# Kernel optimization log

Hardware: AMD Instinct MI355X
Metric: run time of the kernel (lower is better)

## Reference

```python
import jax, jax.numpy as jnp
import numpy as np

B, IN, OUT = 131072, 512, 512


def setup_inputs() -> dict:
    key = jax.random.key(0)
    k1, k2 = jax.random.split(key)
    x = jax.random.normal(k1, (B, IN), dtype=jnp.float32)
    # matches reset_parameters: normal(0, sqrt(1/in_features))
    weight = jax.random.normal(k2, (OUT, IN), dtype=jnp.float32) * jnp.sqrt(1.0 / IN)
    bias = jnp.zeros((OUT,), dtype=jnp.float32)
    return {"x": x, "weight": weight, "bias": bias}


def _binarize(w):
    # deterministic sign binarization: w >= 0 -> +1, else -1
    return jnp.where(w >= 0, 1.0, -1.0).astype(w.dtype)


def reference(x, weight, bias):
    wb = _binarize(weight)            # [out, in], values in {-1, +1}
    # out = x @ wb.T + bias           # [B, out]
    return jnp.einsum("bi,oi->bo", x, wb) + bias
```

## Files before the change

kernel.cpp:

```cpp
#include <hip/hip_runtime.h>
#include <stdint.h>


#define BATCH   131072
#define IN_F    512
#define OUT_F   512
#define BM      64
#define NKT     32

using f32x4  = __attribute__((ext_vector_type(4))) float;
using f32x16 = __attribute__((ext_vector_type(16))) float;
using short8 = __attribute__((ext_vector_type(8))) short;
using usv8   = __attribute__((ext_vector_type(8))) unsigned short;
using u32    = uint32_t;

__global__ void prep_w(const float* __restrict__ W, unsigned short* __restrict__ wf) {
    int t = blockIdx.x * blockDim.x + threadIdx.x;
    int l  = t & 63;
    int nf = (t >> 6) & 15;
    int kt = t >> 10;
    int n = nf * 32 + (l & 31);
    int k = kt * 16 + ((l >> 5) << 3);
    const float* src = W + (size_t)n * IN_F + k;
    f32x4 w0 = *(const f32x4*)(src);
    f32x4 w1 = *(const f32x4*)(src + 4);
    usv8 o;
#pragma unroll
    for (int j = 0; j < 4; ++j) {
        o[j]     = (w0[j] >= 0.0f) ? 0x3F80u : 0xBF80u;
        o[j + 4] = (w1[j] >= 0.0f) ? 0x3F80u : 0xBF80u;
    }
    *(usv8*)(wf + (size_t)t * 8) = o;
}

__global__ __launch_bounds__(512, 4) void gemm_bin(
    const float* __restrict__ X, const unsigned short* __restrict__ WF,
    const float* __restrict__ bias, float* __restrict__ out) {

    __shared__ __align__(16) unsigned short lds[BM * IN_F];

    const int tid  = threadIdx.x;
    const int lane = tid & 63;
    const int wv   = tid >> 6;
    const int m0   = blockIdx.x * BM;

    {
        const int r  = tid >> 3;
        const int sg = tid & 7;
        const float* xr = X + (size_t)(m0 + r) * IN_F;
        char* lrow = (char*)lds + r * 1024;
        const int swz = (r & 7) << 4;
#pragma unroll
        for (int p = 0; p < 8; ++p) {
            const int f0 = sg * 8 + p * 64;
            f32x4 a = *(const f32x4*)(xr + f0);
            f32x4 b = *(const f32x4*)(xr + f0 + 4);
            u32 w0, w1, w2, w3;
            asm("v_cvt_pk_bf16_f32 %0, %1, %2" : "=v"(w0) : "v"(a[0]), "v"(a[1]));
            asm("v_cvt_pk_bf16_f32 %0, %1, %2" : "=v"(w1) : "v"(a[2]), "v"(a[3]));
            asm("v_cvt_pk_bf16_f32 %0, %1, %2" : "=v"(w2) : "v"(b[0]), "v"(b[1]));
            asm("v_cvt_pk_bf16_f32 %0, %1, %2" : "=v"(w3) : "v"(b[2]), "v"(b[3]));
            union { u32 w[4]; usv8 v; } pk;
            pk.w[0] = w0; pk.w[1] = w1; pk.w[2] = w2; pk.w[3] = w3;
            *(usv8*)(lrow + ((sg * 16 + p * 128) ^ swz)) = pk.v;
        }
    }

    f32x16 acc[2][2];
#pragma unroll
    for (int fn = 0; fn < 2; ++fn) {
        const float bv = bias[wv * 64 + fn * 32 + (lane & 31)];
#pragma unroll
        for (int rg = 0; rg < 2; ++rg)
#pragma unroll
            for (int r = 0; r < 16; ++r) acc[rg][fn][r] = bv;
    }
    __syncthreads();

    const int arow  = (lane & 31) * 1024;
    const int ak4   = (lane >> 5) << 4;
    const int aswz  = (lane & 7) << 4;
    const char* lptr = (const char*)lds;
    const short8* wb = (const short8*)(WF) + ((size_t)(wv * 2) * 64 + lane);

#define LDA(dst, kt_)                                                          \
    {                                                                          \
        const int koff_ = ((kt_) * 32 + ak4) ^ aswz;                           \
        _Pragma("unroll")                                                      \
        for (int rg = 0; rg < 2; ++rg)                                         \
            dst[rg] = *(const short8*)(lptr + rg * 32768 + arow + koff_);      \
    }
#define LDB(dst, kt_)                                                          \
    {                                                                          \
        _Pragma("unroll")                                                      \
        for (int fn = 0; fn < 2; ++fn)                                         \
            dst[fn] = wb[(kt_) * 1024 + fn * 64];                              \
    }

    short8 af[2][2], bf[2][2];
    LDA(af[0], 0);
    LDB(bf[0], 0);

#pragma unroll
    for (int kt = 0; kt < NKT; ++kt) {
        const int cur = kt & 1;
        if (kt < NKT - 1) {
            LDB(bf[cur ^ 1], kt + 1);
            LDA(af[cur ^ 1], kt + 1);
        }
#pragma unroll
        for (int rg = 0; rg < 2; ++rg)
#pragma unroll
            for (int fn = 0; fn < 2; ++fn)
                acc[rg][fn] = __builtin_amdgcn_mfma_f32_32x32x16_bf16(
                    af[cur][rg], bf[cur][fn], acc[rg][fn], 0, 0, 0);
    }
#undef LDA
#undef LDB

    const int c     = lane & 31;
    const int rbase = (lane >> 5) << 2;
#pragma unroll
    for (int rg = 0; rg < 2; ++rg)
#pragma unroll
        for (int fn = 0; fn < 2; ++fn)
#pragma unroll
            for (int r = 0; r < 16; ++r) {
                const int row = rg * 32 + (r & 3) + 8 * (r >> 2) + rbase;
                out[(size_t)(m0 + row) * OUT_F + wv * 64 + fn * 32 + c] =
                    acc[rg][fn][r];
            }
}

extern "C" void kernel_launch(void* const* d_in, const int* in_sizes, int n_in,
                              void* d_out, int out_size, void* d_ws, size_t ws_size,
                              hipStream_t stream) {
    const float* X    = (const float*)d_in[0];
    const float* W    = (const float*)d_in[1];
    const float* bias = (const float*)d_in[2];
    float* o          = (float*)d_out;
    unsigned short* wf = (unsigned short*)d_ws;

    hipLaunchKernelGGL(prep_w, dim3(128), dim3(256), 0, stream, W, wf);
    hipLaunchKernelGGL(gemm_bin, dim3(BATCH / BM), dim3(512), 0, stream,
                       X, wf, bias, o);
}
```

Measured before the change: 138.7 us.

## Make GEMM blocks persistent over four row tiles with reused LDS buffer

```diff
diff --git a/kernel.cpp b/kernel.cpp
--- a/kernel.cpp
+++ b/kernel.cpp
@@ -6,6 +6,7 @@
 #define IN_F    512
 #define OUT_F   512
 #define BM      64
+#define NS      4
 #define NKT     32
 
 using f32x4  = __attribute__((ext_vector_type(4))) float;
@@ -33,7 +34,7 @@
     *(usv8*)(wf + (size_t)t * 8) = o;
 }
 
-__global__ __launch_bounds__(512, 4) void gemm_bin(
+__global__ __launch_bounds__(512, 2) void gemm_bin(
     const float* __restrict__ X, const unsigned short* __restrict__ WF,
     const float* __restrict__ bias, float* __restrict__ out) {
 
@@ -42,40 +43,35 @@
     const int tid  = threadIdx.x;
     const int lane = tid & 63;
     const int wv   = tid >> 6;
-    const int m0   = blockIdx.x * BM;
+    const int m0   = blockIdx.x * (NS * BM);
 
-    {
-        const int r  = tid >> 3;
-        const int sg = tid & 7;
-        const float* xr = X + (size_t)(m0 + r) * IN_F;
-        char* lrow = (char*)lds + r * 1024;
-        const int swz = (r & 7) << 4;
-#pragma unroll
-        for (int p = 0; p < 8; ++p) {
-            const int f0 = sg * 8 + p * 64;
-            f32x4 a = *(const f32x4*)(xr + f0);
-            f32x4 b = *(const f32x4*)(xr + f0 + 4);
-            u32 w0, w1, w2, w3;
-            asm("v_cvt_pk_bf16_f32 %0, %1, %2" : "=v"(w0) : "v"(a[0]), "v"(a[1]));
-            asm("v_cvt_pk_bf16_f32 %0, %1, %2" : "=v"(w1) : "v"(a[2]), "v"(a[3]));
-            asm("v_cvt_pk_bf16_f32 %0, %1, %2" : "=v"(w2) : "v"(b[0]), "v"(b[1]));
-            asm("v_cvt_pk_bf16_f32 %0, %1, %2" : "=v"(w3) : "v"(b[2]), "v"(b[3]));
-            union { u32 w[4]; usv8 v; } pk;
-            pk.w[0] = w0; pk.w[1] = w1; pk.w[2] = w2; pk.w[3] = w3;
-            *(usv8*)(lrow + ((sg * 16 + p * 128) ^ swz)) = pk.v;
-        }
+    const int sr  = tid >> 3;
+    const int sg  = tid & 7;
+    char* lrow    = (char*)lds + sr * 1024;
+    const int swz = (sr & 7) << 4;
+
+#define STAGE(s_)                                                              \
+    {                                                                          \
+        const float* xr = X + (size_t)(m0 + (s_) * BM + sr) * IN_F;            \
+        _Pragma("unroll")                                                      \
+        for (int p = 0; p < 8; ++p) {                                          \
+            const int f0 = sg * 8 + p * 64;                                    \
+            f32x4 a = *(const f32x4*)(xr + f0);                                \
+            f32x4 b = *(const f32x4*)(xr + f0 + 4);                            \
+            u32 w0, w1, w2, w3;                                                \
+            asm("v_cvt_pk_bf16_f32 %0, %1, %2" : "=v"(w0)                      \
+                : "v"(a[0]), "v"(a[1]));                                       \
+            asm("v_cvt_pk_bf16_f32 %0, %1, %2" : "=v"(w1)                      \
+                : "v"(a[2]), "v"(a[3]));                                       \
+            asm("v_cvt_pk_bf16_f32 %0, %1, %2" : "=v"(w2)                      \
+                : "v"(b[0]), "v"(b[1]));                                       \
+            asm("v_cvt_pk_bf16_f32 %0, %1, %2" : "=v"(w3)                      \
+                : "v"(b[2]), "v"(b[3]));                                       \
+            union { u32 w[4]; usv8 v; } pk;                                    \
+            pk.w[0] = w0; pk.w[1] = w1; pk.w[2] = w2; pk.w[3] = w3;            \
+            *(usv8*)(lrow + ((sg * 16 + p * 128) ^ swz)) = pk.v;               \
+        }                                                                      \
     }
-
-    f32x16 acc[2][2];
-#pragma unroll
-    for (int fn = 0; fn < 2; ++fn) {
-        const float bv = bias[wv * 64 + fn * 32 + (lane & 31)];
-#pragma unroll
-        for (int rg = 0; rg < 2; ++rg)
-#pragma unroll
-            for (int r = 0; r < 16; ++r) acc[rg][fn][r] = bv;
-    }
-    __syncthreads();
 
     const int arow  = (lane & 31) * 1024;
     const int ak4   = (lane >> 5) << 4;
@@ -86,9 +82,8 @@
 #define LDA(dst, kt_)                                                          \
     {                                                                          \
         const int koff_ = ((kt_) * 32 + ak4) ^ aswz;                           \
-        _Pragma("unroll")                                                      \
-        for (int rg = 0; rg < 2; ++rg)                                         \
-            dst[rg] = *(const short8*)(lptr + rg * 32768 + arow + koff_);      \
+        dst[0] = *(const short8*)(lptr + arow + koff_);                        \
+        dst[1] = *(const short8*)(lptr + arow + 32768 + koff_);                \
     }
 #define LDB(dst, kt_)                                                          \
     {                                                                          \
@@ -97,39 +92,68 @@
             dst[fn] = wb[(kt_) * 1024 + fn * 64];                              \
     }
 
-    short8 af[2][2], bf[2][2];
-    LDA(af[0], 0);
-    LDB(bf[0], 0);
+    const float bv0 = bias[wv * 64 + (lane & 31)];
+    const float bv1 = bias[wv * 64 + 32 + (lane & 31)];
+    const int c     = lane & 31;
+    const int rbase = (lane >> 5) << 2;
 
+    STAGE(0);
+    __syncthreads();
+
+    f32x16 acc[2][2];
+#pragma unroll 1
+    for (int s = 0; s < NS; ++s) {
 #pragma unroll
-    for (int kt = 0; kt < NKT; ++kt) {
-        const int cur = kt & 1;
-        if (kt < NKT - 1) {
-            LDB(bf[cur ^ 1], kt + 1);
-            LDA(af[cur ^ 1], kt + 1);
+        for (int r = 0; r < 16; ++r) {
+            acc[0][0][r] = bv0; acc[0][1][r] = bv1;
+            acc[1][0][r] = bv0; acc[1][1][r] = bv1;
         }
+
+        short8 af[2][2], bf[2][2];
+        LDA(af[0], 0);
+        LDB(bf[0], 0);
+        LDB(bf[1], 1);
 #pragma unroll
-        for (int rg = 0; rg < 2; ++rg)
+        for (int kt = 0; kt < NKT; ++kt) {
+            const int cur = kt & 1;
+            if (kt < NKT - 1) LDA(af[cur ^ 1], kt + 1);
 #pragma unroll
-            for (int fn = 0; fn < 2; ++fn)
-                acc[rg][fn] = __builtin_amdgcn_mfma_f32_32x32x16_bf16(
-                    af[cur][rg], bf[cur][fn], acc[rg][fn], 0, 0, 0);
+            for (int rg = 0; rg < 2; ++rg)
+#pragma unroll
+                for (int fn = 0; fn < 2; ++fn)
+                    acc[rg][fn] = __builtin_amdgcn_mfma_f32_32x32x16_bf16(
+                        af[cur][rg], bf[cur][fn], acc[rg][fn], 0, 0, 0);
+            if (kt < NKT - 2) LDB(bf[cur], kt + 2);
+        }
+
+        {
+            const size_t ms = (size_t)(m0 + s * BM);
+#pragma unroll
+            for (int rg = 0; rg < 2; ++rg)
+#pragma unroll
+                for (int fn = 0; fn < 2; ++fn)
+#pragma unroll
+                    for (int r = 0; r < 16; ++r) {
+                        const int row = rg * 32 + (r & 3) + 8 * (r >> 2) + rbase;
+                        out[(ms + row) * OUT_F + wv * 64 + fn * 32 + c] =
+                            acc[rg][fn][r];
+                    }
+        }
+
+        if (s + 1 < NS) {
+            __builtin_amdgcn_sched_barrier(0);
+            __builtin_amdgcn_s_barrier();
+            __builtin_amdgcn_sched_barrier(0);
+            STAGE(s + 1);
+            asm volatile("s_waitcnt lgkmcnt(0)" ::: "memory");
+            __builtin_amdgcn_sched_barrier(0);
+            __builtin_amdgcn_s_barrier();
+            __builtin_amdgcn_sched_barrier(0);
+        }
     }
+#undef STAGE
 #undef LDA
 #undef LDB
-
-    const int c     = lane & 31;
-    const int rbase = (lane >> 5) << 2;
-#pragma unroll
-    for (int rg = 0; rg < 2; ++rg)
-#pragma unroll
-        for (int fn = 0; fn < 2; ++fn)
-#pragma unroll
-            for (int r = 0; r < 16; ++r) {
-                const int row = rg * 32 + (r & 3) + 8 * (r >> 2) + rbase;
-                out[(size_t)(m0 + row) * OUT_F + wv * 64 + fn * 32 + c] =
-                    acc[rg][fn][r];
-            }
 }
 
 extern "C" void kernel_launch(void* const* d_in, const int* in_sizes, int n_in,
@@ -142,6 +166,6 @@
     unsigned short* wf = (unsigned short*)d_ws;
 
     hipLaunchKernelGGL(prep_w, dim3(128), dim3(256), 0, stream, W, wf);
-    hipLaunchKernelGGL(gemm_bin, dim3(BATCH / BM), dim3(512), 0, stream,
+    hipLaunchKernelGGL(gemm_bin, dim3(BATCH / (BM * NS)), dim3(512), 0, stream,
                        X, wf, bias, o);
 }
```

Result: slower. 270.1 us (+94.8%).
